# Performance work log

Measured on AMD Instinct MI355X. Metric: run time of the kernel, lower is better.

The kernel has to match this reference:

```python
import jax, jax.numpy as jnp
import numpy as np

B, D, U, BR, IU, HID = 1024, 2048, 4096, 4, 3072, 32


def setup_inputs() -> dict:
    key = jax.random.key(0)
    ks = jax.random.split(key, 12)
    inputs = jax.random.normal(ks[0], (B, D), dtype=jnp.float32)
    # dendritic kernel / bias / delay (glorot-ish scale)
    w = jax.random.normal(ks[1], (D, U, BR), dtype=jnp.float32) * 0.02
    b = jax.random.normal(ks[2], (U, BR), dtype=jnp.float32) * 0.01
    delay = jax.random.normal(ks[3], (D, U, BR), dtype=jnp.float32) * 0.5
    # branch gating dense (softmax applied in reference)
    Wg = jax.random.normal(ks[4], (D, BR), dtype=jnp.float32) * 0.02
    bg = jnp.zeros((BR,), dtype=jnp.float32)
    # DynamicConnectivity attention net: Dense(32, relu) -> Dense(U, sigmoid)
    W1 = jax.random.normal(ks[5], (U, HID), dtype=jnp.float32) * 0.02
    b1 = jnp.zeros((HID,), dtype=jnp.float32)
    W2 = jax.random.normal(ks[6], (HID, U), dtype=jnp.float32) * 0.02
    b2 = jnp.zeros((U,), dtype=jnp.float32)
    # non-trainable state
    neuron_mask = jnp.concatenate([jnp.ones((IU,), jnp.float32), jnp.zeros((U - IU,), jnp.float32)])
    neuron_activation_avg = jax.random.uniform(ks[7], (U,), dtype=jnp.float32) * 0.1
    return {"inputs": inputs, "w": w, "b": b, "delay": delay, "Wg": Wg, "bg": bg,
            "W1": W1, "b1": b1, "W2": W2, "b2": b2,
            "neuron_mask": neuron_mask, "neuron_activation_avg": neuron_activation_avg}


def reference(inputs, w, b, delay, Wg, bg, W1, b1, W2, b2, neuron_mask, neuron_activation_avg):
    # sigmoid-gated weights, 3-way tensordot -> [B, U, BR]
    w_mod = w * jax.nn.sigmoid(delay)
    branch_outputs = jnp.einsum('bd,duk->buk', inputs, w_mod) + b
    # per-branch softmax gating from the input, soft combine over branches
    gating = jax.nn.softmax(inputs @ Wg + bg, axis=-1)            # [B, BR]
    z_combined = jnp.einsum('buk,bk->bu', branch_outputs, gating)  # [B, U]
    # dynamic connectivity from neuron activation EMA state: [1, U]
    h = jax.nn.relu(neuron_activation_avg[None, :] @ W1 + b1)
    connectivity = jax.nn.sigmoid(h @ W2 + b2)                     # [1, U]
    z_modulated = z_combined * connectivity * neuron_mask[None, :]
    a = jax.nn.relu(z_modulated)
    return a
```

## Files before the change

kernel.cpp:

```cpp
#include <hip/hip_runtime.h>
#include <cstdint>
#include <cstddef>

typedef __bf16 bf16;
typedef __bf16 bf16x4 __attribute__((ext_vector_type(4)));
typedef __bf16 bf16x8 __attribute__((ext_vector_type(8)));
typedef float f32x4 __attribute__((ext_vector_type(4)));

#define B_SZ 1024
#define D_SZ 2048
#define U_SZ 4096
#define BR_SZ 4
#define N_SZ (U_SZ * BR_SZ)

#define WS_WT 0
#define WS_A (64u * 1024u * 1024u)
#define WS_GAT (WS_A + 4u * 1024u * 1024u)
#define WS_H (WS_GAT + 16384u)

__device__ __forceinline__ float sigmoidf_(float x) { return 1.f / (1.f + __expf(-x)); }

__device__ __forceinline__ uint32_t pack2_(float lo, float hi) {
  union { bf16 h[2]; uint32_t u; } cv;
  cv.h[0] = (bf16)lo; cv.h[1] = (bf16)hi;
  return cv.u;
}

__global__ void k01_prep(const float* __restrict__ in, bf16* __restrict__ wa,
                         const float* __restrict__ Wg, const float* __restrict__ bg,
                         float* __restrict__ gat, float* __restrict__ wsh) {
  int row = blockIdx.x, tid = threadIdx.x;
  if (row == 0 && tid < 32) wsh[tid] = 0.f;
  const float* ir = in + (size_t)row * D_SZ;
  float a0 = 0, a1 = 0, a2 = 0, a3 = 0;
#pragma unroll
  for (int c = 0; c < 2; c++) {
    int d = c * 1024 + tid * 4;
    float4 x = *(const float4*)(ir + d);
    bf16x4 o;
    o[0] = (bf16)x.x; o[1] = (bf16)x.y; o[2] = (bf16)x.z; o[3] = (bf16)x.w;
    *(bf16x4*)(wa + ((size_t)(d >> 6) * B_SZ + row) * 64 + (d & 63)) = o;
    const float xs[4] = {x.x, x.y, x.z, x.w};
#pragma unroll
    for (int j = 0; j < 4; j++) {
      float4 wg = ((const float4*)Wg)[d + j];
      a0 += xs[j] * wg.x; a1 += xs[j] * wg.y; a2 += xs[j] * wg.z; a3 += xs[j] * wg.w;
    }
  }
#pragma unroll
  for (int off = 32; off; off >>= 1) {
    a0 += __shfl_down(a0, off); a1 += __shfl_down(a1, off);
    a2 += __shfl_down(a2, off); a3 += __shfl_down(a3, off);
  }
  __shared__ float red[4][4];
  int wv = tid >> 6, ln = tid & 63;
  if (ln == 0) { red[wv][0] = a0; red[wv][1] = a1; red[wv][2] = a2; red[wv][3] = a3; }
  __syncthreads();
  if (tid == 0) {
    float s0 = red[0][0] + red[1][0] + red[2][0] + red[3][0] + bg[0];
    float s1 = red[0][1] + red[1][1] + red[2][1] + red[3][1] + bg[1];
    float s2 = red[0][2] + red[1][2] + red[2][2] + red[3][2] + bg[2];
    float s3 = red[0][3] + red[1][3] + red[2][3] + red[3][3] + bg[3];
    float m = fmaxf(fmaxf(s0, s1), fmaxf(s2, s3));
    float e0 = __expf(s0 - m), e1 = __expf(s1 - m), e2 = __expf(s2 - m), e3 = __expf(s3 - m);
    float inv = 1.f / (e0 + e1 + e2 + e3);
    ((float4*)gat)[row] = make_float4(e0 * inv, e1 * inv, e2 * inv, e3 * inv);
  }
}

__global__ void k2a_h(const float* __restrict__ avg, const float* __restrict__ W1,
                      float* __restrict__ wsh) {
  int t = threadIdx.x;
  int h = t & 31, seg = t >> 5;
  int u0 = blockIdx.x * 64 + seg * 8;
  float p = 0.f;
#pragma unroll
  for (int j = 0; j < 8; j++) {
    int u = u0 + j;
    p += avg[u] * W1[u * 32 + h];
  }
  __shared__ float red[8][32];
  red[seg][h] = p;
  __syncthreads();
  if (t < 32) {
    float s = 0.f;
#pragma unroll
    for (int sg = 0; sg < 8; sg++) s += red[sg][t];
    atomicAdd(&wsh[t], s);
  }
}

#define K3P 66
__global__ __launch_bounds__(256) void k3_wmod_t(const float* __restrict__ w,
                                                 const float* __restrict__ delay,
                                                 bf16* __restrict__ wt) {
  __shared__ uint32_t buf[64 * K3P];
  int tid = threadIdx.x;
  int n0 = blockIdx.x * 64;
  int d0 = blockIdx.y * 128;
  int n4 = tid & 15, dh = tid >> 4;

  float4 wv[8], dv[8];
  const float* wp = w + (size_t)(d0 + dh * 8) * N_SZ + n0 + n4 * 4;
  const float* dp = delay + (size_t)(d0 + dh * 8) * N_SZ + n0 + n4 * 4;
#pragma unroll
  for (int k = 0; k < 8; k++) {
    wv[k] = *(const float4*)(wp + (size_t)k * N_SZ);
    dv[k] = *(const float4*)(dp + (size_t)k * N_SZ);
  }
#pragma unroll
  for (int k2 = 0; k2 < 4; k2++) {
    const float* f0 = (const float*)&wv[2 * k2];
    const float* f1 = (const float*)&wv[2 * k2 + 1];
    const float* g0 = (const float*)&dv[2 * k2];
    const float* g1 = (const float*)&dv[2 * k2 + 1];
#pragma unroll
    for (int j = 0; j < 4; j++) {
      float lo = f0[j] * sigmoidf_(g0[j]);
      float hi = f1[j] * sigmoidf_(g1[j]);
      buf[(n4 * 4 + j) * K3P + dh * 4 + k2] = pack2_(lo, hi);
    }
  }
  __syncthreads();
  int n = tid >> 2, seg = tid & 3;
  const uint32_t* r = &buf[n * K3P + seg * 16];
  bf16* dst = wt + ((size_t)((d0 >> 6) + (seg >> 1)) * N_SZ + n0 + n) * 64 + (seg & 1) * 32;
#pragma unroll
  for (int q = 0; q < 4; q++) {
    uint4 v;
    v.x = r[q * 4 + 0]; v.y = r[q * 4 + 1]; v.z = r[q * 4 + 2]; v.w = r[q * 4 + 3];
    *(uint4*)(dst + q * 8) = v;
  }
}

__global__ __launch_bounds__(256, 2) void k4_gemm(
    const bf16* __restrict__ A, const bf16* __restrict__ Bt,
    const float* __restrict__ gating, const float* __restrict__ bias,
    const float* __restrict__ wsh, const float* __restrict__ b1,
    const float* __restrict__ W2, const float* __restrict__ b2,
    const float* __restrict__ mask, float* __restrict__ out) {
  __shared__ bf16 Al[128 * 64];
  __shared__ bf16 Bl[128 * 64];
  __shared__ float gat[128 * 4];
  __shared__ float conn_l[32];
  int tid = threadIdx.x;
  int lane = tid & 63, wave = tid >> 6;
  int bid = blockIdx.x;
  int xcd = bid & 7, p = bid >> 3;
  int mt = p & 7, nt = (xcd << 4) | (p >> 3);
  int m0 = mt * 128, n0 = nt * 128;
  int wm = (wave & 1) * 64, wn = (wave >> 1) * 64;
  int quad = lane >> 4, row16 = lane & 15;
  int r7 = row16 & 7;

  f32x4 acc[4][4];
  const f32x4 z4 = {0.f, 0.f, 0.f, 0.f};
#pragma unroll
  for (int i = 0; i < 4; i++)
#pragma unroll
    for (int j = 0; j < 4; j++) acc[i][j] = z4;

  if (tid < 128) *(float4*)&gat[tid * 4] = *(const float4*)&gating[(m0 + tid) * 4];
  if (tid < 32) {
    int u = (n0 >> 2) + tid;
    float s = b2[u];
#pragma unroll
    for (int h = 0; h < 32; h++) s += fmaxf(wsh[h] + b1[h], 0.f) * W2[h * U_SZ + u];
    conn_l[tid] = sigmoidf_(s) * mask[u];
  }

  int srow = lane >> 3;
  int scol = ((lane & 7) ^ srow) * 8;
  for (int kt = 0; kt < 32; kt++) {
#pragma unroll
    for (int c = 0; c < 4; c++) {
      int rb = wave * 32 + c * 8;
      const bf16* ga = A + ((size_t)kt * B_SZ + m0 + rb + srow) * 64 + scol;
      __builtin_amdgcn_global_load_lds(
          (const __attribute__((address_space(1))) void*)ga,
          (__attribute__((address_space(3))) void*)(Al + rb * 64), 16, 0, 0);
      const bf16* gb = Bt + ((size_t)kt * N_SZ + n0 + rb + srow) * 64 + scol;
      __builtin_amdgcn_global_load_lds(
          (const __attribute__((address_space(1))) void*)gb,
          (__attribute__((address_space(3))) void*)(Bl + rb * 64), 16, 0, 0);
    }
    __syncthreads();
#pragma unroll
    for (int kk = 0; kk < 64; kk += 32) {
      int csw = (((kk >> 3) + quad) ^ r7) * 8;
      bf16x8 af[4], bfr[4];
#pragma unroll
      for (int i = 0; i < 4; i++)
        af[i] = *(const bf16x8*)&Al[(wm + i * 16 + row16) * 64 + csw];
#pragma unroll
      for (int j = 0; j < 4; j++)
        bfr[j] = *(const bf16x8*)&Bl[(wn + j * 16 + row16) * 64 + csw];
#pragma unroll
      for (int i = 0; i < 4; i++)
#pragma unroll
        for (int j = 0; j < 4; j++)
          acc[i][j] = __builtin_amdgcn_mfma_f32_16x16x32_bf16(af[i], bfr[j], acc[i][j], 0, 0, 0);
    }
    __syncthreads();
  }

  int k = lane & 3;
#pragma unroll
  for (int j = 0; j < 4; j++) {
    int n_l = wn + j * 16 + row16;
    int n_g = n0 + n_l;
    int u = n_g >> 2;
    float bv = bias[n_g];
    float cv = conn_l[n_l >> 2];
#pragma unroll
    for (int i = 0; i < 4; i++) {
#pragma unroll
      for (int r = 0; r < 4; r++) {
        int r_l = wm + i * 16 + quad * 4 + r;
        float g = gat[r_l * 4 + k];
        float v = (acc[i][j][r] + bv) * g;
        v += __shfl_xor(v, 1);
        v += __shfl_xor(v, 2);
        if (k == 0) out[(size_t)(m0 + r_l) * U_SZ + u] = fmaxf(v * cv, 0.f);
      }
    }
  }
}

extern "C" void kernel_launch(void* const* d_in, const int* in_sizes, int n_in,
                              void* d_out, int out_size, void* d_ws, size_t ws_size,
                              hipStream_t stream) {
  const float* inputs = (const float*)d_in[0];
  const float* w = (const float*)d_in[1];
  const float* bb = (const float*)d_in[2];
  const float* delay = (const float*)d_in[3];
  const float* Wg = (const float*)d_in[4];
  const float* bg = (const float*)d_in[5];
  const float* W1 = (const float*)d_in[6];
  const float* b1 = (const float*)d_in[7];
  const float* W2 = (const float*)d_in[8];
  const float* b2 = (const float*)d_in[9];
  const float* mask = (const float*)d_in[10];
  const float* avg = (const float*)d_in[11];
  float* out = (float*)d_out;
  char* ws = (char*)d_ws;
  bf16* wt = (bf16*)(ws + WS_WT);
  bf16* wa = (bf16*)(ws + WS_A);
  float* gat = (float*)(ws + WS_GAT);
  float* wsh = (float*)(ws + WS_H);

  hipLaunchKernelGGL(k01_prep, dim3(B_SZ), dim3(256), 0, stream, inputs, wa, Wg, bg, gat, wsh);
  hipLaunchKernelGGL(k2a_h, dim3(U_SZ / 64), dim3(256), 0, stream, avg, W1, wsh);
  hipLaunchKernelGGL(k3_wmod_t, dim3(N_SZ / 64, D_SZ / 128), dim3(256), 0, stream, w, delay, wt);
  hipLaunchKernelGGL(k4_gemm, dim3((B_SZ / 128) * (N_SZ / 128)), dim3(256), 0, stream, wa, wt, gat, bb, wsh, b1, W2, b2, mask, out);
}
```

Measured before the change: 396.1 us.

## Fold hidden-layer reduction into prep kernel and retile weight-modulation transpose

The small avg@W1 reduction moves into an extra block of the prep kernel, so one launch and the atomics are gone. That single block loops serially over 512 elements per thread, which may lengthen the prep kernel's tail. The sigmoid-weight transpose kernel is retiled to 256 columns by 64 rows, reading a full 64-row K slab per block. Each thread now writes one complete 128-byte row with nontemporal stores, aiming for better global write coalescing and less cache pollution before the GEMM.

```diff
diff --git a/kernel.cpp b/kernel.cpp
--- a/kernel.cpp
+++ b/kernel.cpp
@@ -6,6 +6,7 @@
 typedef __bf16 bf16x4 __attribute__((ext_vector_type(4)));
 typedef __bf16 bf16x8 __attribute__((ext_vector_type(8)));
 typedef float f32x4 __attribute__((ext_vector_type(4)));
+typedef uint32_t u32x4 __attribute__((ext_vector_type(4)));
 
 #define B_SZ 1024
 #define D_SZ 2048
@@ -28,9 +29,28 @@
 
 __global__ void k01_prep(const float* __restrict__ in, bf16* __restrict__ wa,
                          const float* __restrict__ Wg, const float* __restrict__ bg,
-                         float* __restrict__ gat, float* __restrict__ wsh) {
+                         float* __restrict__ gat, float* __restrict__ wsh,
+                         const float* __restrict__ avg, const float* __restrict__ W1) {
   int row = blockIdx.x, tid = threadIdx.x;
-  if (row == 0 && tid < 32) wsh[tid] = 0.f;
+  if (row == 1024) {
+    int h = tid & 31, seg = tid >> 5;
+    float p = 0.f;
+    int u0 = seg * 512;
+    for (int j = 0; j < 512; j++) {
+      int u = u0 + j;
+      p += avg[u] * W1[u * 32 + h];
+    }
+    __shared__ float red[8][32];
+    red[seg][h] = p;
+    __syncthreads();
+    if (tid < 32) {
+      float s = 0.f;
+#pragma unroll
+      for (int sg = 0; sg < 8; sg++) s += red[sg][tid];
+      wsh[tid] = s;
+    }
+    return;
+  }
   const float* ir = in + (size_t)row * D_SZ;
   float a0 = 0, a1 = 0, a2 = 0, a3 = 0;
 #pragma unroll
@@ -52,15 +72,15 @@
     a0 += __shfl_down(a0, off); a1 += __shfl_down(a1, off);
     a2 += __shfl_down(a2, off); a3 += __shfl_down(a3, off);
   }
-  __shared__ float red[4][4];
+  __shared__ float red2[4][4];
   int wv = tid >> 6, ln = tid & 63;
-  if (ln == 0) { red[wv][0] = a0; red[wv][1] = a1; red[wv][2] = a2; red[wv][3] = a3; }
+  if (ln == 0) { red2[wv][0] = a0; red2[wv][1] = a1; red2[wv][2] = a2; red2[wv][3] = a3; }
   __syncthreads();
   if (tid == 0) {
-    float s0 = red[0][0] + red[1][0] + red[2][0] + red[3][0] + bg[0];
-    float s1 = red[0][1] + red[1][1] + red[2][1] + red[3][1] + bg[1];
-    float s2 = red[0][2] + red[1][2] + red[2][2] + red[3][2] + bg[2];
-    float s3 = red[0][3] + red[1][3] + red[2][3] + red[3][3] + bg[3];
+    float s0 = red2[0][0] + red2[1][0] + red2[2][0] + red2[3][0] + bg[0];
+    float s1 = red2[0][1] + red2[1][1] + red2[2][1] + red2[3][1] + bg[1];
+    float s2 = red2[0][2] + red2[1][2] + red2[2][2] + red2[3][2] + bg[2];
+    float s3 = red2[0][3] + red2[1][3] + red2[2][3] + red2[3][3] + bg[3];
     float m = fmaxf(fmaxf(s0, s1), fmaxf(s2, s3));
     float e0 = __expf(s0 - m), e1 = __expf(s1 - m), e2 = __expf(s2 - m), e3 = __expf(s3 - m);
     float inv = 1.f / (e0 + e1 + e2 + e3);
@@ -68,68 +88,41 @@
   }
 }
 
-__global__ void k2a_h(const float* __restrict__ avg, const float* __restrict__ W1,
-                      float* __restrict__ wsh) {
-  int t = threadIdx.x;
-  int h = t & 31, seg = t >> 5;
-  int u0 = blockIdx.x * 64 + seg * 8;
-  float p = 0.f;
-#pragma unroll
-  for (int j = 0; j < 8; j++) {
-    int u = u0 + j;
-    p += avg[u] * W1[u * 32 + h];
-  }
-  __shared__ float red[8][32];
-  red[seg][h] = p;
-  __syncthreads();
-  if (t < 32) {
-    float s = 0.f;
-#pragma unroll
-    for (int sg = 0; sg < 8; sg++) s += red[sg][t];
-    atomicAdd(&wsh[t], s);
-  }
-}
-
-#define K3P 66
+#define K3_PITCH 260
 __global__ __launch_bounds__(256) void k3_wmod_t(const float* __restrict__ w,
                                                  const float* __restrict__ delay,
                                                  bf16* __restrict__ wt) {
-  __shared__ uint32_t buf[64 * K3P];
+  __shared__ uint32_t buf[32 * K3_PITCH];
   int tid = threadIdx.x;
-  int n0 = blockIdx.x * 64;
-  int d0 = blockIdx.y * 128;
-  int n4 = tid & 15, dh = tid >> 4;
-
-  float4 wv[8], dv[8];
-  const float* wp = w + (size_t)(d0 + dh * 8) * N_SZ + n0 + n4 * 4;
-  const float* dp = delay + (size_t)(d0 + dh * 8) * N_SZ + n0 + n4 * 4;
-#pragma unroll
-  for (int k = 0; k < 8; k++) {
-    wv[k] = *(const float4*)(wp + (size_t)k * N_SZ);
-    dv[k] = *(const float4*)(dp + (size_t)k * N_SZ);
-  }
-#pragma unroll
-  for (int k2 = 0; k2 < 4; k2++) {
-    const float* f0 = (const float*)&wv[2 * k2];
-    const float* f1 = (const float*)&wv[2 * k2 + 1];
-    const float* g0 = (const float*)&dv[2 * k2];
-    const float* g1 = (const float*)&dv[2 * k2 + 1];
-#pragma unroll
-    for (int j = 0; j < 4; j++) {
-      float lo = f0[j] * sigmoidf_(g0[j]);
-      float hi = f1[j] * sigmoidf_(g1[j]);
-      buf[(n4 * 4 + j) * K3P + dh * 4 + k2] = pack2_(lo, hi);
-    }
+  int lane = tid & 63, wave = tid >> 6;
+  int n0 = blockIdx.x * 256;
+  int d0 = blockIdx.y * 64;
+  const float* wb = w + (size_t)(d0 + wave * 16) * N_SZ + n0 + lane * 4;
+  const float* db = delay + (size_t)(d0 + wave * 16) * N_SZ + n0 + lane * 4;
+#pragma unroll
+  for (int s = 0; s < 8; s++) {
+    float4 w0 = *(const float4*)(wb + (size_t)(2 * s) * N_SZ);
+    float4 w1 = *(const float4*)(wb + (size_t)(2 * s + 1) * N_SZ);
+    float4 e0 = *(const float4*)(db + (size_t)(2 * s) * N_SZ);
+    float4 e1 = *(const float4*)(db + (size_t)(2 * s + 1) * N_SZ);
+    u32x4 pk;
+    pk.x = pack2_(w0.x * sigmoidf_(e0.x), w1.x * sigmoidf_(e1.x));
+    pk.y = pack2_(w0.y * sigmoidf_(e0.y), w1.y * sigmoidf_(e1.y));
+    pk.z = pack2_(w0.z * sigmoidf_(e0.z), w1.z * sigmoidf_(e1.z));
+    pk.w = pack2_(w0.w * sigmoidf_(e0.w), w1.w * sigmoidf_(e1.w));
+    *(u32x4*)&buf[(wave * 8 + s) * K3_PITCH + lane * 4] = pk;
   }
   __syncthreads();
-  int n = tid >> 2, seg = tid & 3;
-  const uint32_t* r = &buf[n * K3P + seg * 16];
-  bf16* dst = wt + ((size_t)((d0 >> 6) + (seg >> 1)) * N_SZ + n0 + n) * 64 + (seg & 1) * 32;
-#pragma unroll
-  for (int q = 0; q < 4; q++) {
-    uint4 v;
-    v.x = r[q * 4 + 0]; v.y = r[q * 4 + 1]; v.z = r[q * 4 + 2]; v.w = r[q * 4 + 3];
-    *(uint4*)(dst + q * 8) = v;
+  uint32_t col[32];
+#pragma unroll
+  for (int dp = 0; dp < 32; dp++) col[dp] = buf[dp * K3_PITCH + tid];
+  bf16* dst = wt + ((size_t)(d0 >> 6) * N_SZ + n0 + tid) * 64;
+#pragma unroll
+  for (int q = 0; q < 8; q++) {
+    u32x4 v;
+    v.x = col[q * 4 + 0]; v.y = col[q * 4 + 1];
+    v.z = col[q * 4 + 2]; v.w = col[q * 4 + 3];
+    __builtin_nontemporal_store(v, (u32x4*)(dst + q * 8));
   }
 }
 
@@ -249,8 +242,7 @@
   float* gat = (float*)(ws + WS_GAT);
   float* wsh = (float*)(ws + WS_H);
 
-  hipLaunchKernelGGL(k01_prep, dim3(B_SZ), dim3(256), 0, stream, inputs, wa, Wg, bg, gat, wsh);
-  hipLaunchKernelGGL(k2a_h, dim3(U_SZ / 64), dim3(256), 0, stream, avg, W1, wsh);
-  hipLaunchKernelGGL(k3_wmod_t, dim3(N_SZ / 64, D_SZ / 128), dim3(256), 0, stream, w, delay, wt);
+  hipLaunchKernelGGL(k01_prep, dim3(B_SZ + 1), dim3(256), 0, stream, inputs, wa, Wg, bg, gat, wsh, avg, W1);
+  hipLaunchKernelGGL(k3_wmod_t, dim3(N_SZ / 256, D_SZ / 64), dim3(256), 0, stream, w, delay, wt);
   hipLaunchKernelGGL(k4_gemm, dim3((B_SZ / 128) * (N_SZ / 128)), dim3(256), 0, stream, wa, wt, gat, bb, wsh, b1, W2, b2, mask, out);
 }
```

After: 538.5 us. +36.0%, slower.
